# Performance work log

Measured on AMD Instinct MI355X. Metric: run time of the kernel, lower is better.

The kernel has to match this reference:

```python
import jax, jax.numpy as jnp
import numpy as np

EPS = 1e-6
K = 32
NUM_RBF = 16
NUM_PE = 16
SCALE = 30.0


def _norm(x, axis=-1):
    n = jnp.linalg.norm(x, axis=axis, keepdims=True)
    return x / jnp.maximum(n, 1e-12)


def _ln(x, g, b):
    # torch.var default is unbiased (ddof=1)
    mu = x.mean(-1, keepdims=True)
    sig = jnp.sqrt(x.var(-1, keepdims=True, ddof=1) + EPS)
    return g * (x - mu) / (sig + EPS) + b


def _gather_nodes(nodes, idx):
    # nodes [B,N,C], idx [B,N,K] -> [B,N,K,C]
    return jax.vmap(lambda nd, ei: nd[ei])(nodes, idx)


def _quat(R):
    # R [B,N,K,3,3] -> unit quaternion [B,N,K,4]
    diag = jnp.diagonal(R, axis1=-2, axis2=-1)
    Rxx, Ryy, Rzz = diag[..., 0], diag[..., 1], diag[..., 2]
    mag = 0.5 * jnp.sqrt(jnp.abs(1.0 + jnp.stack(
        [Rxx - Ryy - Rzz, -Rxx + Ryy - Rzz, -Rxx - Ryy + Rzz], -1)))
    sgn = jnp.sign(jnp.stack(
        [R[..., 2, 1] - R[..., 1, 2], R[..., 0, 2] - R[..., 2, 0], R[..., 1, 0] - R[..., 0, 1]], -1))
    w = jnp.sqrt(jax.nn.relu(1.0 + diag.sum(-1, keepdims=True))) / 2.0
    return _norm(jnp.concatenate([sgn * mag, w], -1))


def _orient(X, E_idx):
    # backbone frames + relative orientation features ('coarse')
    B = X.shape[0]
    dX = X[:, 1:] - X[:, :-1]
    U = _norm(dX)
    u2, u1, u0 = U[:, :-2], U[:, 1:-1], U[:, 2:]
    n2 = _norm(jnp.cross(u2, u1))
    n1 = _norm(jnp.cross(u1, u0))
    cosA = jnp.clip(-(u1 * u0).sum(-1), -1 + EPS, 1 - EPS)
    A = jnp.arccos(cosA)
    cosD = jnp.clip((n2 * n1).sum(-1), -1 + EPS, 1 - EPS)
    Dih = jnp.sign((u2 * n1).sum(-1)) * jnp.arccos(cosD)
    AD = jnp.stack([jnp.cos(A), jnp.sin(A) * jnp.cos(Dih), jnp.sin(A) * jnp.sin(Dih)], -1)
    AD = jnp.pad(AD, ((0, 0), (1, 2), (0, 0)))  # [B,N,3]
    o1 = _norm(u2 - u1)
    Of = jnp.stack([o1, n2, jnp.cross(o1, n2)], 2).reshape(B, -1, 9)
    Of = jnp.pad(Of, ((0, 0), (1, 2), (0, 0)))  # [B,N,9]
    O_nb = _gather_nodes(Of, E_idx).reshape(*E_idx.shape, 3, 3)
    X_nb = _gather_nodes(X, E_idx)
    Om = Of.reshape(B, -1, 3, 3)
    dU = _norm(jnp.einsum('bnij,bnkj->bnki', Om, X_nb - X[:, :, None, :]))
    R = jnp.einsum('bnji,bnkjl->bnkil', Om, O_nb)  # O^T @ O_neighbors
    return AD, jnp.concatenate([dU, _quat(R)], -1)  # [B,N,3], [B,N,K,7]


def _forward(X, mask, Wn, bn, gn, hn, We, be, ge, he, Wv, bv, Wq, bq,
             lW1, lb1, lW2, lb2, lW3, lb3, lWi, lbi, lWo, lbo, lg0, lh0, lg1, lh1):
    B, N, _ = X.shape
    # ---- kNN graph: pairwise dist + topk (smallest) ----
    mask2 = mask[:, None, :] * mask[:, :, None]
    dX = X[:, None, :, :] - X[:, :, None, :]
    D = mask2 * jnp.sqrt((dX * dX).sum(-1) + EPS)
    D_adj = D + (1.0 - mask2) * D.max(-1, keepdims=True)
    negD, E_idx = jax.lax.top_k(-D_adj, K)
    D_nb = -negD  # [B,N,K]
    # ---- edge features: positional encodings + RBF + orientations ----
    ii = jnp.arange(N, dtype=jnp.float32)[None, :, None]
    d = (E_idx.astype(jnp.float32) - ii)[..., None]
    freq = jnp.exp(jnp.arange(0, NUM_PE, 2, dtype=jnp.float32) * (-np.log(10000.0) / NUM_PE))
    ang = d * freq
    E_pos = jnp.concatenate([jnp.cos(ang), jnp.sin(ang)], -1)  # [B,N,K,16]
    mu = jnp.linspace(0.0, 20.0, NUM_RBF)
    RBF = jnp.exp(-(((D_nb[..., None] - mu) * (NUM_RBF / 20.0)) ** 2))  # [B,N,K,16]
    AD, O_feat = _orient(X, E_idx)
    # ---- embed + normalize ----
    V = _ln(AD @ Wn + bn, gn, hn)
    E = jnp.concatenate([E_pos, RBF, O_feat], -1)  # [B,N,K,39]
    E = _ln(E @ We + be, ge, he)
    h_V = V @ Wv + bv
    h_E = E @ Wq + bq
    m_att = mask[:, :, None] * _gather_nodes(mask[..., None], E_idx)[..., 0]
    # ---- MPNN layers: gather -> concat -> 3-layer MLP -> mask -> sum ----
    for l in range(lW1.shape[0]):
        h_EV = jnp.concatenate([
            jnp.broadcast_to(h_V[:, :, None, :], h_E.shape),
            h_E,
            _gather_nodes(h_V, E_idx)], -1)  # [B,N,K,3H]
        msg = jax.nn.relu(h_EV @ lW1[l] + lb1[l])
        msg = jax.nn.relu(msg @ lW2[l] + lb2[l])
        msg = (msg @ lW3[l] + lb3[l]) * m_att[..., None]
        h_V = _ln(h_V + msg.sum(-2) / SCALE, lg0[l], lh0[l])
        dh = jax.nn.relu(h_V @ lWi[l] + lbi[l]) @ lWo[l] + lbo[l]
        h_V = _ln(h_V + dh, lg1[l], lh1[l])
        h_V = mask[..., None] * h_V
    return h_V


def setup_inputs() -> dict:
    key = jax.random.key(0)
    ks = iter(jax.random.split(key, 32))
    def rn(shape, fan_in):
        return jax.random.normal(next(ks), shape, dtype=jnp.float32) / np.float32(np.sqrt(fan_in))
    H, Dff, L = 128, 512, 3
    inp = {}
    inp['X'] = jax.random.normal(next(ks), (2, 2048, 3), dtype=jnp.float32)
    inp['mask'] = jnp.ones((2, 2048), jnp.float32)
    inp['Wn'] = rn((3, H), 3);   inp['bn'] = jnp.zeros(H)
    inp['gn'] = jnp.ones(H);     inp['hn'] = jnp.zeros(H)
    inp['We'] = rn((39, H), 39); inp['be'] = jnp.zeros(H)
    inp['ge'] = jnp.ones(H);     inp['he'] = jnp.zeros(H)
    inp['Wv'] = rn((H, H), H);   inp['bv'] = jnp.zeros(H)
    inp['Wq'] = rn((H, H), H);   inp['bq'] = jnp.zeros(H)
    inp['lW1'] = rn((L, 3 * H, H), 3 * H); inp['lb1'] = jnp.zeros((L, H))
    inp['lW2'] = rn((L, H, H), H);         inp['lb2'] = jnp.zeros((L, H))
    inp['lW3'] = rn((L, H, H), H);         inp['lb3'] = jnp.zeros((L, H))
    inp['lWi'] = rn((L, H, Dff), H);       inp['lbi'] = jnp.zeros((L, Dff))
    inp['lWo'] = rn((L, Dff, H), Dff);     inp['lbo'] = jnp.zeros((L, H))
    inp['lg0'] = jnp.ones((L, H));         inp['lh0'] = jnp.zeros((L, H))
    inp['lg1'] = jnp.ones((L, H));         inp['lh1'] = jnp.zeros((L, H))
    return inp


def reference(X, mask, Wn, bn, gn, hn, We, be, ge, he, Wv, bv, Wq, bq,
              lW1, lb1, lW2, lb2, lW3, lb3, lWi, lbi, lWo, lbo, lg0, lh0, lg1, lh1):
    return _forward(X, mask, Wn, bn, gn, hn, We, be, ge, he, Wv, bv, Wq, bq,
                    lW1, lb1, lW2, lb2, lW3, lb3, lWi, lbi, lWo, lbo, lg0, lh0, lg1, lh1)
```

## Files before the change

### kernel.cpp

```cpp
#include <hip/hip_runtime.h>
#include <math.h>

typedef __attribute__((ext_vector_type(8))) short short8;
typedef __attribute__((ext_vector_type(4))) float f32x4;

#define BB 2
#define NN 2048
#define KK 32
#define HH 128
#define DFF 512
#define EPSF 1e-6f
#define INFV 1e30f

#define KNN_BLK 1024
#define PACK_BLK 2656
#define ORIENT_BLK 16

#define MFMA16(a, b, c) __builtin_amdgcn_mfma_f32_16x16x32_bf16((a), (b), (c), 0, 0, 0)


__device__ __forceinline__ unsigned short f2bf(float f) {
    unsigned u = __float_as_uint(f);
    u += 0x7fffu + ((u >> 16) & 1u);
    return (unsigned short)(u >> 16);
}

__device__ __forceinline__ float bf2f(unsigned short h) {
    return __uint_as_float(((unsigned)h) << 16);
}

__device__ __forceinline__ void f2bf2(float x, short& hi, short& lo) {
    unsigned short h = f2bf(x);
    hi = (short)h;
    lo = (short)f2bf(x - bf2f(h));
}

__device__ __forceinline__ short8 cvt8h(f32x4 a, f32x4 b) {
    short8 h8;
    #pragma unroll
    for (int i = 0; i < 4; i++) h8[i] = (short)f2bf(a[i]);
    #pragma unroll
    for (int i = 0; i < 4; i++) h8[4 + i] = (short)f2bf(b[i]);
    return h8;
}

__device__ __forceinline__ float sgnf(float x) {
    return (x > 0.f) ? 1.f : ((x < 0.f) ? -1.f : 0.f);
}

__device__ __forceinline__ void norm3(float& x, float& y, float& z) {
    float n = sqrtf(x * x + y * y + z * z);
    n = fmaxf(n, 1e-12f);
    x /= n; y /= n; z /= n;
}


__device__ void knn_body(int bid4, const float* __restrict__ X,
                         const float* __restrict__ mask,
                         int* __restrict__ E_idx,
                         float* __restrict__ D_nb) {
    int w = threadIdx.x >> 6, lane = threadIdx.x & 63;
    int g = bid4 * 4 + w;
    int b = g >> 11, n = g & 2047;
    const float* Xb = X + (size_t)b * NN * 3;
    const float* mb = mask + (size_t)b * NN;

    float xn0 = Xb[n * 3], xn1 = Xb[n * 3 + 1], xn2 = Xb[n * 3 + 2];
    float mn = mb[n];

    float Dv[32], m2a[32];
    float lmax = -1e30f;
    #pragma unroll
    for (int s = 0; s < 32; s++) {
        int j = s * 64 + lane;
        float dx = Xb[j * 3] - xn0, dy = Xb[j * 3 + 1] - xn1, dz = Xb[j * 3 + 2] - xn2;
        float d = sqrtf(dx * dx + dy * dy + dz * dz + EPSF);
        float m2 = mn * mb[j];
        float v = m2 * d;
        Dv[s] = v; m2a[s] = m2;
        lmax = fmaxf(lmax, v);
    }
    #pragma unroll
    for (int off = 1; off <= 32; off <<= 1) lmax = fmaxf(lmax, __shfl_xor(lmax, off));
    float Dmax = lmax;
    #pragma unroll
    for (int s = 0; s < 32; s++) Dv[s] += (1.f - m2a[s]) * Dmax;

    float l1 = INFV, l2 = INFV; int s1 = 0, s2 = 0;
    #pragma unroll
    for (int s = 0; s < 32; s++) {
        float v = Dv[s];
        bool lt1 = v < l1;
        bool lt2 = v < l2;
        float o1 = l1; int os1 = s1;
        l1 = lt1 ? v : l1;  s1 = lt1 ? s : s1;
        l2 = lt1 ? o1 : (lt2 ? v : l2);
        s2 = lt1 ? os1 : (lt2 ? s : s2);
    }

    unsigned used = 0u;
    float keepd = 0.f; int keepj = 0;

    for (int s = 0; s < KK; s++) {
        float m = l1;
        #pragma unroll
        for (int off = 1; off <= 32; off <<= 1) m = fminf(m, __shfl_xor(m, off));
        unsigned long long ball = __ballot(l1 == m);
        int jwin;
        if (__popcll(ball) == 1) {
            int src = (int)(__ffsll((long long)ball) - 1);
            jwin = __shfl(s1 * 64 + lane, src);
        } else {
            int jme = (l1 == m) ? (s1 * 64 + lane) : 0x7FFFFFFF;
            jwin = jme;
            #pragma unroll
            for (int off = 1; off <= 32; off <<= 1) jwin = min(jwin, __shfl_xor(jwin, off));
        }
        if (lane == s) { keepd = m; keepj = jwin; }
        if (lane == (jwin & 63)) {
            used |= 1u << s1;
            l1 = l2; s1 = s2;
            l2 = INFV;
            if (l1 >= INFV) {
                l1 = INFV; l2 = INFV;
                #pragma unroll
                for (int i = 0; i < 32; i++) {
                    float v = ((used >> i) & 1u) ? INFV : Dv[i];
                    bool lt1 = v < l1;
                    bool lt2 = v < l2;
                    float o1 = l1; int os1 = s1;
                    l1 = lt1 ? v : l1;  s1 = lt1 ? i : s1;
                    l2 = lt1 ? o1 : (lt2 ? v : l2);
                    s2 = lt1 ? os1 : (lt2 ? i : s2);
                }
            }
        }
    }
    if (lane < KK) {
        E_idx[(size_t)g * KK + lane] = keepj;
        D_nb[(size_t)g * KK + lane] = keepd;
    }
}

__device__ __forceinline__ void packB(const float* __restrict__ src, short* __restrict__ dH,
                                      short* __restrict__ dL, int e, int KC, int N, int Kreal) {
    int j = e & 7, ln = (e >> 3) & 63, t = e >> 9;
    int kc = t % KC, nt = t / KC;
    int k = kc * 32 + (ln >> 4) * 8 + j;
    int n = nt * 16 + (ln & 15);
    float v = (k < Kreal) ? src[(size_t)k * N + n] : 0.f;
    short hi, lo; f2bf2(v, hi, lo);
    dH[e] = hi; dL[e] = lo;
}

__device__ void pack_body(int e,
                          const float* __restrict__ We, const float* __restrict__ Wq,
                          const float* __restrict__ lW1, const float* __restrict__ lW2,
                          const float* __restrict__ lW3, const float* __restrict__ lWi,
                          const float* __restrict__ lWo, const float* __restrict__ Wv,
                          short* __restrict__ WeP, short* __restrict__ WqP,
                          short* __restrict__ W1bP, short* __restrict__ W2P,
                          short* __restrict__ W3P, short* __restrict__ WiP,
                          short* __restrict__ WoP, short* __restrict__ W1acP,
                          short* __restrict__ WvP) {
    if (e < 8192) { packB(We, WeP, WeP + 8192, e, 2, 128, 39); return; }
    e -= 8192;
    if (e < 16384) { packB(Wq, WqP, WqP + 16384, e, 4, 128, 128); return; }
    e -= 16384;
    if (e < 49152) {
        int l = e >> 14, r = e & 16383;
        packB(lW1 + (size_t)l * 49152 + 16384, W1bP + l * 32768, W1bP + l * 32768 + 16384, r, 4, 128, 128);
        return;
    }
    e -= 49152;
    if (e < 49152) {
        int l = e >> 14, r = e & 16383;
        packB(lW2 + (size_t)l * 16384, W2P + l * 32768, W2P + l * 32768 + 16384, r, 4, 128, 128);
        return;
    }
    e -= 49152;
    if (e < 49152) {
        int l = e >> 14, r = e & 16383;
        packB(lW3 + (size_t)l * 16384, W3P + l * 32768, W3P + l * 32768 + 16384, r, 4, 128, 128);
        return;
    }
    e -= 49152;
    if (e < 196608) {
        int l = e / 65536, r = e % 65536;
        packB(lWi + (size_t)l * 65536, WiP + l * 131072, WiP + l * 131072 + 65536, r, 4, 512, 128);
        return;
    }
    e -= 196608;
    if (e < 196608) {
        int l = e / 65536, r = e % 65536;
        packB(lWo + (size_t)l * 65536, WoP + l * 131072, WoP + l * 131072 + 65536, r, 16, 128, 512);
        return;
    }
    e -= 196608;
    if (e < 98304) {
        int l = e / 32768, r = e % 32768;
        int j = r & 7, ln = (r >> 3) & 63, t = r >> 9;
        int kc = t & 3, nt = t >> 2;
        int k = kc * 32 + (ln >> 4) * 8 + j;
        int n = nt * 16 + (ln & 15);
        const float* base = lW1 + (size_t)l * 49152;
        float v = (n < 128) ? base[(size_t)k * 128 + n] : base[(size_t)(256 + k) * 128 + (n - 128)];
        short hi, lo; f2bf2(v, hi, lo);
        short* dH = W1acP + l * 65536;
        dH[r] = hi; dH[32768 + r] = lo;
        return;
    }
    e -= 98304;
    packB(Wv, WvP, WvP + 16384, e, 4, 128, 128);
}

__device__ void orient_body(int t, const float* __restrict__ X,
                            float* __restrict__ AD, float* __restrict__ Of) {
    if (t >= BB * NN) return;
    int b = t / NN, n = t % NN;
    float* ad = AD + (size_t)t * 3;
    float* of = Of + (size_t)t * 9;
    if (n < 1 || n > NN - 3) {
        ad[0] = ad[1] = ad[2] = 0.f;
        #pragma unroll
        for (int i = 0; i < 9; i++) of[i] = 0.f;
        return;
    }
    const float* Xb = X + (size_t)b * NN * 3;
    float p0x = Xb[(n - 1) * 3], p0y = Xb[(n - 1) * 3 + 1], p0z = Xb[(n - 1) * 3 + 2];
    float p1x = Xb[n * 3],       p1y = Xb[n * 3 + 1],       p1z = Xb[n * 3 + 2];
    float p2x = Xb[(n + 1) * 3], p2y = Xb[(n + 1) * 3 + 1], p2z = Xb[(n + 1) * 3 + 2];
    float p3x = Xb[(n + 2) * 3], p3y = Xb[(n + 2) * 3 + 1], p3z = Xb[(n + 2) * 3 + 2];

    float u2x = p1x - p0x, u2y = p1y - p0y, u2z = p1z - p0z; norm3(u2x, u2y, u2z);
    float u1x = p2x - p1x, u1y = p2y - p1y, u1z = p2z - p1z; norm3(u1x, u1y, u1z);
    float u0x = p3x - p2x, u0y = p3y - p2y, u0z = p3z - p2z; norm3(u0x, u0y, u0z);

    float n2x = u2y * u1z - u2z * u1y, n2y = u2z * u1x - u2x * u1z, n2z = u2x * u1y - u2y * u1x;
    norm3(n2x, n2y, n2z);
    float n1x = u1y * u0z - u1z * u0y, n1y = u1z * u0x - u1x * u0z, n1z = u1x * u0y - u1y * u0x;
    norm3(n1x, n1y, n1z);

    float cosA = -(u1x * u0x + u1y * u0y + u1z * u0z);
    cosA = fminf(fmaxf(cosA, -1.f + EPSF), 1.f - EPSF);
    float A = acosf(cosA);
    float cosD = n2x * n1x + n2y * n1y + n2z * n1z;
    cosD = fminf(fmaxf(cosD, -1.f + EPSF), 1.f - EPSF);
    float sg = sgnf(u2x * n1x + u2y * n1y + u2z * n1z);
    float Dih = sg * acosf(cosD);

    ad[0] = cosf(A);
    ad[1] = sinf(A) * cosf(Dih);
    ad[2] = sinf(A) * sinf(Dih);

    float o1x = u2x - u1x, o1y = u2y - u1y, o1z = u2z - u1z; norm3(o1x, o1y, o1z);
    float cx = o1y * n2z - o1z * n2y, cy = o1z * n2x - o1x * n2z, cz = o1x * n2y - o1y * n2x;
    of[0] = o1x; of[1] = o1y; of[2] = o1z;
    of[3] = n2x; of[4] = n2y; of[5] = n2z;
    of[6] = cx;  of[7] = cy;  of[8] = cz;
}


__global__ __launch_bounds__(256) void front_kernel(const float* __restrict__ X,
                                                    const float* __restrict__ mask,
                                                    int* __restrict__ E_idx,
                                                    float* __restrict__ D_nb,
                                                    const float* __restrict__ We,
                                                    const float* __restrict__ Wq,
                                                    const float* __restrict__ lW1,
                                                    const float* __restrict__ lW2,
                                                    const float* __restrict__ lW3,
                                                    const float* __restrict__ lWi,
                                                    const float* __restrict__ lWo,
                                                    const float* __restrict__ Wv,
                                                    short* __restrict__ WeP,
                                                    short* __restrict__ WqP,
                                                    short* __restrict__ W1bP,
                                                    short* __restrict__ W2P,
                                                    short* __restrict__ W3P,
                                                    short* __restrict__ WiP,
                                                    short* __restrict__ WoP,
                                                    short* __restrict__ W1acP,
                                                    short* __restrict__ WvP,
                                                    float* __restrict__ ADb,
                                                    float* __restrict__ Ofb) {
    int blk = blockIdx.x;
    if (blk < KNN_BLK) {
        knn_body(blk, X, mask, E_idx, D_nb);
    } else if (blk < KNN_BLK + PACK_BLK) {
        pack_body((blk - KNN_BLK) * 256 + threadIdx.x,
                  We, Wq, lW1, lW2, lW3, lWi, lWo, Wv,
                  WeP, WqP, W1bP, W2P, W3P, WiP, WoP, W1acP, WvP);
    } else {
        orient_body((blk - KNN_BLK - PACK_BLK) * 256 + threadIdx.x, X, ADb, Ofb);
    }
}


__global__ __launch_bounds__(128) void mid_kernel(const float* __restrict__ X,
                                                  const int* __restrict__ E_idx,
                                                  const float* __restrict__ D_nb,
                                                  const float* __restrict__ Of,
                                                  const float* __restrict__ be,
                                                  const float* __restrict__ ge,
                                                  const float* __restrict__ he,
                                                  const float* __restrict__ bq,
                                                  const short* __restrict__ WeP,
                                                  const short* __restrict__ WqP,
                                                  unsigned short* __restrict__ hEbH,
                                                  const float* __restrict__ AD,
                                                  const float* __restrict__ Wn,
                                                  const float* __restrict__ bn,
                                                  const float* __restrict__ gn,
                                                  const float* __restrict__ hn,
                                                  const short* __restrict__ WvP,
                                                  const float* __restrict__ bv,
                                                  const short* __restrict__ W1acP0,
                                                  const float* __restrict__ b1_0,
                                                  float* __restrict__ hV,
                                                  float* __restrict__ P,
                                                  float* __restrict__ Q) {
    __shared__ __align__(16) char smemRaw[15872];

    if (blockIdx.x < (unsigned)(BB * NN)) {
        short* AefH = (short*)smemRaw;
        short* AeH  = (short*)(smemRaw + 4608);
        float* beS  = (float*)(smemRaw + 13312);
        float* geS  = beS + HH;
        float* heS  = geS + HH;
        float* bqS  = heS + HH;
        float* redSe = (float*)(smemRaw + 15360);

        int bid = blockIdx.x; int b = bid >> 11, n = bid & 2047; int tid = threadIdx.x;
        int lane = tid & 63, w = tid >> 6;
        beS[tid] = be[tid]; geS[tid] = ge[tid]; heS[tid] = he[tid]; bqS[tid] = bq[tid];
        {
            unsigned* Az = (unsigned*)AefH;
            for (int i = tid; i < 32 * 72 / 2; i += 128) Az[i] = 0u;
        }
        __syncthreads();

        int part = tid >> 5, k = tid & 31;
        int e = E_idx[(size_t)bid * KK + k];
        float dpos = (float)e - (float)n;
        if (part == 1 || part == 2) {
            int p0 = (part - 1) * 4;
            #pragma unroll
            for (int p = 0; p < 4; p++) {
                float fr = (part == 1)
                    ? ((p == 0) ? 1.f : (p == 1) ? 0.31622776601683794f
                       : (p == 2) ? 0.1f : 0.031622776601683791f)
                    : ((p == 0) ? 0.01f : (p == 1) ? 0.0031622776601683794f
                       : (p == 2) ? 0.001f : 0.00031622776601683794f);
                float ang = dpos * fr;
                AefH[k * 72 + p0 + p]     = (short)f2bf(__cosf(ang));
                AefH[k * 72 + 8 + p0 + p] = (short)f2bf(__sinf(ang));
            }
        } else if (part == 3) {
            float Dv = D_nb[(size_t)bid * KK + k];
            #pragma unroll
            for (int i = 0; i < 16; i++) {
                float m = (20.f / 15.f) * (float)i;
                float z = (Dv - m) * 0.8f;
                AefH[k * 72 + 16 + i] = (short)f2bf(__expf(-z * z));
            }
        } else {
            const float* Omp = Of + (size_t)(b * NN + n) * 9;
            const float* Onp = Of + (size_t)(b * NN + e) * 9;
            float Om[9], On[9];
            #pragma unroll
            for (int i = 0; i < 9; i++) { Om[i] = Omp[i]; On[i] = Onp[i]; }
            float vx = X[(size_t)(b * NN + e) * 3 + 0] - X[(size_t)(b * NN + n) * 3 + 0];
            float vy = X[(size_t)(b * NN + e) * 3 + 1] - X[(size_t)(b * NN + n) * 3 + 1];
            float vz = X[(size_t)(b * NN + e) * 3 + 2] - X[(size_t)(b * NN + n) * 3 + 2];
            float t0 = Om[0] * vx + Om[1] * vy + Om[2] * vz;
            float t1 = Om[3] * vx + Om[4] * vy + Om[5] * vz;
            float t2 = Om[6] * vx + Om[7] * vy + Om[8] * vz;
            float nr = fmaxf(sqrtf(t0 * t0 + t1 * t1 + t2 * t2), 1e-12f);
            AefH[k * 72 + 32] = (short)f2bf(t0 / nr);
            AefH[k * 72 + 33] = (short)f2bf(t1 / nr);
            AefH[k * 72 + 34] = (short)f2bf(t2 / nr);
            float R[9];
            #pragma unroll
            for (int i = 0; i < 3; i++)
                #pragma unroll
                for (int l = 0; l < 3; l++)
                    R[i * 3 + l] = Om[0 + i] * On[0 + l] + Om[3 + i] * On[3 + l] + Om[6 + i] * On[6 + l];
            float Rxx = R[0], Ryy = R[4], Rzz = R[8];
            float mx = 0.5f * sqrtf(fabsf(1.f + Rxx - Ryy - Rzz));
            float my = 0.5f * sqrtf(fabsf(1.f - Rxx + Ryy - Rzz));
            float mz = 0.5f * sqrtf(fabsf(1.f - Rxx - Ryy + Rzz));
            float qx = sgnf(R[7] - R[5]) * mx;
            float qy = sgnf(R[2] - R[6]) * my;
            float qz = sgnf(R[3] - R[1]) * mz;
            float qw = 0.5f * sqrtf(fmaxf(1.f + Rxx + Ryy + Rzz, 0.f));
            float qn = fmaxf(sqrtf(qx * qx + qy * qy + qz * qz + qw * qw), 1e-12f);
            AefH[k * 72 + 35] = (short)f2bf(qx / qn);
            AefH[k * 72 + 36] = (short)f2bf(qy / qn);
            AefH[k * 72 + 37] = (short)f2bf(qz / qn);
            AefH[k * 72 + 38] = (short)f2bf(qw / qn);
        }
        __syncthreads();

        int m = lane & 15, q = lane >> 4;
        short8 aW[2][2];
        #pragma unroll
        for (int t = 0; t < 2; t++) {
            int row = (t * 16 + m) * 72;
            aW[t][0] = *(const short8*)&AefH[row + q * 8];
            aW[t][1] = *(const short8*)&AefH[row + 32 + q * 8];
        }
        f32x4 accA[4][2];
        #pragma unroll
        for (int nt4 = 0; nt4 < 4; nt4++) {
            int ntg = w * 4 + nt4;
            const short* B0 = &WeP[((ntg * 2 + 0) * 64 + lane) * 8];
            const short* B1 = &WeP[((ntg * 2 + 1) * 64 + lane) * 8];
            short8 b0h = *(const short8*)B0, b0l = *(const short8*)(B0 + 8192);
            short8 b1h = *(const short8*)B1, b1l = *(const short8*)(B1 + 8192);
            float bc = beS[ntg * 16 + m];
            #pragma unroll
            for (int t = 0; t < 2; t++) {
                f32x4 acc = {bc, bc, bc, bc};
                acc = MFMA16(aW[t][0], b0h, acc);
                acc = MFMA16(aW[t][0], b0l, acc);
                acc = MFMA16(aW[t][1], b1h, acc);
                acc = MFMA16(aW[t][1], b1l, acc);
                accA[nt4][t] = acc;
            }
        }
        #pragma unroll
        for (int t = 0; t < 2; t++)
            #pragma unroll
            for (int r = 0; r < 4; r++) {
                float su = accA[0][t][r] + accA[1][t][r] + accA[2][t][r] + accA[3][t][r];
                float sq2 = accA[0][t][r] * accA[0][t][r] + accA[1][t][r] * accA[1][t][r]
                          + accA[2][t][r] * accA[2][t][r] + accA[3][t][r] * accA[3][t][r];
                #pragma unroll
                for (int off = 1; off <= 8; off <<= 1) {
                    su += __shfl_xor(su, off); sq2 += __shfl_xor(sq2, off);
                }
                if (m == 0) {
                    int row = t * 16 + q * 4 + r;
                    redSe[(w * 2 + 0) * 32 + row] = su;
                    redSe[(w * 2 + 1) * 32 + row] = sq2;
                }
            }
        __syncthreads();
        float muA[2][4], invA[2][4];
        #pragma unroll
        for (int t = 0; t < 2; t++)
            #pragma unroll
            for (int r = 0; r < 4; r++) {
                int row = t * 16 + q * 4 + r;
                float S  = redSe[0 * 32 + row] + redSe[2 * 32 + row];
                float Q2 = redSe[1 * 32 + row] + redSe[3 * 32 + row];
                float mu = S * (1.f / HH);
                float var = (Q2 - (float)HH * mu * mu) * (1.f / (HH - 1));
                muA[t][r] = mu;
                invA[t][r] = 1.f / (sqrtf(var + EPSF) + EPSF);
            }
        #pragma unroll
        for (int nt4 = 0; nt4 < 4; nt4++) {
            int col = (w * 4 + nt4) * 16 + m;
            float g = geS[col], hh = heS[col];
            #pragma unroll
            for (int t = 0; t < 2; t++)
                #pragma unroll
                for (int r = 0; r < 4; r++) {
                    int edge = t * 16 + q * 4 + r;
                    float y = g * (accA[nt4][t][r] - muA[t][r]) * invA[t][r] + hh;
                    AeH[edge * 136 + col] = (short)f2bf(y);
                }
        }
        __syncthreads();

        short8 ah[2][4];
        #pragma unroll
        for (int t = 0; t < 2; t++)
            #pragma unroll
            for (int kc = 0; kc < 4; kc++)
                ah[t][kc] = *(const short8*)&AeH[(t * 16 + m) * 136 + kc * 32 + q * 8];
        #pragma unroll
        for (int nt4 = 0; nt4 < 4; nt4++) {
            int ntg = w * 4 + nt4;
            int col = ntg * 16 + m;
            short8 qh[4], ql[4];
            #pragma unroll
            for (int kc = 0; kc < 4; kc++) {
                const short* Bp = &WqP[((ntg * 4 + kc) * 64 + lane) * 8];
                qh[kc] = *(const short8*)Bp;
                ql[kc] = *(const short8*)(Bp + 16384);
            }
            float bc = bqS[col];
            #pragma unroll
            for (int t = 0; t < 2; t++) {
                f32x4 acc = {bc, bc, bc, bc};
                #pragma unroll
                for (int kc = 0; kc < 4; kc++) {
                    acc = MFMA16(ah[t][kc], qh[kc], acc);
                    acc = MFMA16(ah[t][kc], ql[kc], acc);
                }
                #pragma unroll
                for (int r = 0; r < 4; r++) {
                    int edge = t * 16 + q * 4 + r;
                    hEbH[(size_t)bid * (KK * HH) + edge * HH + col] = f2bf(acc[r]);
                }
            }
        }
    } else {
        short* yH  = (short*)smemRaw;
        short* hvH = (short*)(smemRaw + 4352);

        int nb = blockIdx.x - BB * NN;
        int g0 = nb * 16;
        int tid = threadIdx.x;
        int lane = tid & 63, w = tid >> 6;
        int m = lane & 15, q = lane >> 4;

        {
            int i = tid >> 3;
            int j = tid & 7;
            int h0 = j * 16;
            const float* ad = AD + (size_t)(g0 + i) * 3;
            float a0 = ad[0], a1 = ad[1], a2 = ad[2];
            float v[16];
            float su = 0.f, sq = 0.f;
            #pragma unroll
            for (int c = 0; c < 16; c++) {
                int h = h0 + c;
                float t = bn[h] + a0 * Wn[h] + a1 * Wn[HH + h] + a2 * Wn[2 * HH + h];
                v[c] = t; su += t; sq += t * t;
            }
            #pragma unroll
            for (int off = 1; off <= 4; off <<= 1) {
                su += __shfl_xor(su, off); sq += __shfl_xor(sq, off);
            }
            float mu = su * (1.f / HH);
            float var = (sq - (float)HH * mu * mu) * (1.f / (HH - 1));
            float inv = 1.f / (sqrtf(var + EPSF) + EPSF);
            #pragma unroll
            for (int c = 0; c < 16; c++) {
                int h = h0 + c;
                yH[i * 136 + h] = (short)f2bf(gn[h] * (v[c] - mu) * inv + hn[h]);
            }
        }
        __syncthreads();

        short8 ayh[4];
        #pragma unroll
        for (int kc = 0; kc < 4; kc++)
            ayh[kc] = *(const short8*)&yH[m * 136 + kc * 32 + q * 8];
        #pragma unroll
        for (int u = 0; u < 4; u++) {
            int nt = w * 4 + u;
            int col = nt * 16 + m;
            float bc = bv[col];
            f32x4 a = {bc, bc, bc, bc};
            #pragma unroll
            for (int kc = 0; kc < 4; kc++) {
                const short* Bp = &WvP[((nt * 4 + kc) * 64 + lane) * 8];
                short8 bh = *(const short8*)Bp, bl = *(const short8*)(Bp + 16384);
                a = MFMA16(ayh[kc], bh, a);
                a = MFMA16(ayh[kc], bl, a);
            }
            #pragma unroll
            for (int r = 0; r < 4; r++) {
                int rw = q * 4 + r;
                hV[(size_t)(g0 + rw) * HH + col] = a[r];
                hvH[rw * 136 + col] = (short)f2bf(a[r]);
            }
        }
        __syncthreads();

        short8 avh[4];
        #pragma unroll
        for (int kc = 0; kc < 4; kc++)
            avh[kc] = *(const short8*)&hvH[m * 136 + kc * 32 + q * 8];
        #pragma unroll
        for (int u = 0; u < 8; u++) {
            int nt = w * 8 + u;
            int col = nt * 16 + m;
            float b0 = (nt < 8) ? b1_0[col] : 0.f;
            f32x4 a = {b0, b0, b0, b0};
            #pragma unroll
            for (int kc = 0; kc < 4; kc++) {
                const short* Bp = &W1acP0[((nt * 4 + kc) * 64 + lane) * 8];
                short8 bh = *(const short8*)Bp, bl = *(const short8*)(Bp + 32768);
                a = MFMA16(avh[kc], bh, a);
                a = MFMA16(avh[kc], bl, a);
            }
            #pragma unroll
            for (int r = 0; r < 4; r++) {
                size_t rw = g0 + q * 4 + r;
                if (nt < 8) P[rw * HH + col] = a[r];
                else        Q[rw * HH + (col - 128)] = a[r];
            }
        }
    }
}


__global__ __launch_bounds__(128) void msg_kernel(const float* __restrict__ mask,
                                                  const int* __restrict__ E_idx,
                                                  const unsigned short* __restrict__ hEbH,
                                                  const float* __restrict__ P,
                                                  const float* __restrict__ Q,
                                                  const short* __restrict__ W1bP,
                                                  const short* __restrict__ W2P,
                                                  const float* __restrict__ b2,
                                                  float* __restrict__ sOut,
                                                  float* __restrict__ cntOut) {
    __shared__ short stg[2][32 * 136];
    __shared__ short AmH[2][32 * 136];

    int tid = threadIdx.x;
    int w = tid >> 6, lane = tid & 63;
    int gA = blockIdx.x * 2;
    int b = gA >> 11;
    int m = lane & 15, q = lane >> 4;

    {
        const short8* src = (const short8*)(hEbH + (size_t)gA * (KK * HH));
        #pragma unroll
        for (int it = 0; it < 8; it++) {
            int idx = it * 128 + tid;
            int nd = idx >> 9;
            int rem = idx & 511;
            int e = rem >> 4;
            int c8 = rem & 15;
            short8 v = src[idx];
            *(short8*)&stg[nd][e * 136 + c8 * 8] = v;
        }
    }

    int qbase[2][2][4]; float mt[2][2][4];
    #pragma unroll
    for (int nd = 0; nd < 2; nd++) {
        float maskv = mask[gA + nd];
        #pragma unroll
        for (int t = 0; t < 2; t++)
            #pragma unroll
            for (int r = 0; r < 4; r++) {
                int row = t * 16 + q * 4 + r;
                int e = E_idx[(size_t)(gA + nd) * KK + row];
                qbase[nd][t][r] = (b * NN + e) * HH;
                mt[nd][t][r] = maskv * mask[b * NN + e];
            }
    }
    {
        float c8 = mt[w][0][0] + mt[w][0][1] + mt[w][0][2] + mt[w][0][3]
                 + mt[w][1][0] + mt[w][1][1] + mt[w][1][2] + mt[w][1][3];
        c8 += __shfl_xor(c8, 16);
        c8 += __shfl_xor(c8, 32);
        if (lane == 0) cntOut[gA + w] = c8;
    }

    float preg[2][4], b2reg[4];
    #pragma unroll
    for (int nt4 = 0; nt4 < 4; nt4++) {
        int colg = (w * 4 + nt4) * 16 + m;
        b2reg[nt4] = b2[colg];
        preg[0][nt4] = P[(size_t)gA * HH + colg];
        preg[1][nt4] = P[(size_t)(gA + 1) * HH + colg];
    }
    __syncthreads();

    #pragma unroll
    for (int nt4 = 0; nt4 < 4; nt4++) {
        int ntg = w * 4 + nt4;
        int colg = ntg * 16 + m;
        short8 bh[4], bl[4];
        #pragma unroll
        for (int kc = 0; kc < 4; kc++) {
            const short* Bp = &W1bP[((ntg * 4 + kc) * 64 + lane) * 8];
            bh[kc] = *(const short8*)Bp;
            bl[kc] = *(const short8*)(Bp + 16384);
        }
        #pragma unroll
        for (int nd = 0; nd < 2; nd++) {
            f32x4 t0 = {0.f, 0.f, 0.f, 0.f}, t1 = {0.f, 0.f, 0.f, 0.f};
            #pragma unroll
            for (int kc = 0; kc < 4; kc++) {
                short8 a0 = *(const short8*)&stg[nd][(0 * 16 + m) * 136 + kc * 32 + q * 8];
                short8 a1 = *(const short8*)&stg[nd][(1 * 16 + m) * 136 + kc * 32 + q * 8];
                t0 = MFMA16(a0, bh[kc], t0);
                t0 = MFMA16(a0, bl[kc], t0);
                t1 = MFMA16(a1, bh[kc], t1);
                t1 = MFMA16(a1, bl[kc], t1);
            }
            float pp = preg[nd][nt4];
            #pragma unroll
            for (int r = 0; r < 4; r++) {
                float v0 = fmaxf(t0[r] + pp + Q[(size_t)qbase[nd][0][r] + colg], 0.f);
                AmH[nd][(q * 4 + r) * 136 + colg] = (short)f2bf(v0);
                float v1 = fmaxf(t1[r] + pp + Q[(size_t)qbase[nd][1][r] + colg], 0.f);
                AmH[nd][(16 + q * 4 + r) * 136 + colg] = (short)f2bf(v1);
            }
        }
    }
    __syncthreads();

    #pragma unroll
    for (int nt4 = 0; nt4 < 4; nt4++) {
        int ntg = w * 4 + nt4;
        short8 bh[4], bl[4];
        #pragma unroll
        for (int kc = 0; kc < 4; kc++) {
            const short* Bp = &W2P[((ntg * 4 + kc) * 64 + lane) * 8];
            bh[kc] = *(const short8*)Bp;
            bl[kc] = *(const short8*)(Bp + 16384);
        }
        float bc = b2reg[nt4];
        #pragma unroll
        for (int nd = 0; nd < 2; nd++) {
            f32x4 a0 = {bc, bc, bc, bc}, a1 = {bc, bc, bc, bc};
            #pragma unroll
            for (int kc = 0; kc < 4; kc++) {
                short8 m0 = *(const short8*)&AmH[nd][(0 * 16 + m) * 136 + kc * 32 + q * 8];
                short8 m1 = *(const short8*)&AmH[nd][(1 * 16 + m) * 136 + kc * 32 + q * 8];
                a0 = MFMA16(m0, bh[kc], a0);
                a0 = MFMA16(m0, bl[kc], a0);
                a1 = MFMA16(m1, bh[kc], a1);
                a1 = MFMA16(m1, bl[kc], a1);
            }
            float part = 0.f;
            #pragma unroll
            for (int r = 0; r < 4; r++)
                part += fmaxf(a0[r], 0.f) * mt[nd][0][r] + fmaxf(a1[r], 0.f) * mt[nd][1][r];
            part += __shfl_xor(part, 16);
            part += __shfl_xor(part, 32);
            if (q == 0) sOut[(size_t)(gA + nd) * HH + ntg * 16 + m] = part;
        }
    }
}


#define HSTR 520

__global__ __launch_bounds__(256, 3) void node_kernel(const float* __restrict__ mask,
                                                      const float* __restrict__ sbuf,
                                                      const float* __restrict__ cntb,
                                                      const float* __restrict__ hVin,
                                                      const short* __restrict__ W3P,
                                                      const float* __restrict__ b3,
                                                      const short* __restrict__ WiP,
                                                      const float* __restrict__ biN,
                                                      const short* __restrict__ WoP,
                                                      const float* __restrict__ boN,
                                                      const float* __restrict__ g0,
                                                      const float* __restrict__ h0,
                                                      const float* __restrict__ g1,
                                                      const float* __restrict__ h1,
                                                      const short* __restrict__ W1P,
                                                      const float* __restrict__ b1n,
                                                      float* __restrict__ hVout,
                                                      float* __restrict__ Pn,
                                                      float* __restrict__ Qn) {
    __shared__ short rbH[16 * 136];
    __shared__ short hbH[16 * HSTR];
    __shared__ float redS[4][2][16];
    __shared__ float g0S[128], h0S[128], g1S[128], h1S[128], b3S[128], boS[128], b1S[128];
    __shared__ float biS[512];

    int tid = threadIdx.x;
    int w = tid >> 6, lane = tid & 63;
    int m = lane & 15, q = lane >> 4;
    int rowT = blockIdx.x * 16;

    for (int i = tid; i < 128; i += 256) {
        g0S[i] = g0[i]; h0S[i] = h0[i]; g1S[i] = g1[i]; h1S[i] = h1[i];
        b3S[i] = b3[i]; boS[i] = boN[i]; b1S[i] = W1P ? b1n[i] : 0.f;
    }
    for (int i = tid; i < 512; i += 256) biS[i] = biN[i];
    __syncthreads();

    short8 ash[4];
    #pragma unroll
    for (int kc = 0; kc < 4; kc++) {
        const float* sp = &sbuf[(size_t)(rowT + m) * HH + kc * 32 + q * 8];
        f32x4 x0 = *(const f32x4*)sp;
        f32x4 x1 = *(const f32x4*)(sp + 4);
        ash[kc] = cvt8h(x0, x1);
    }
    float cntr[4];
    #pragma unroll
    for (int r = 0; r < 4; r++) cntr[r] = cntb[rowT + q * 4 + r];

    f32x4 vC2[2];
    #pragma unroll
    for (int t = 0; t < 2; t++) {
        int nt = 2 * w + t;
        f32x4 a = {0.f, 0.f, 0.f, 0.f};
        #pragma unroll
        for (int kc = 0; kc < 4; kc++) {
            const short* Bp = &W3P[((nt * 4 + kc) * 64 + lane) * 8];
            short8 bh = *(const short8*)Bp, bl = *(const short8*)(Bp + 16384);
            a = MFMA16(ash[kc], bh, a);
            a = MFMA16(ash[kc], bl, a);
        }
        int col = nt * 16 + m;
        #pragma unroll
        for (int r = 0; r < 4; r++) {
            float tv = (a[r] + cntr[r] * b3S[col]) * (1.f / 30.f);
            a[r] = hVin[(size_t)(rowT + q * 4 + r) * HH + col] + tv;
        }
        vC2[t] = a;
    }

    {
        float su[4] = {0, 0, 0, 0}, sq[4] = {0, 0, 0, 0};
        #pragma unroll
        for (int t = 0; t < 2; t++)
            #pragma unroll
            for (int r = 0; r < 4; r++) { float v = vC2[t][r]; su[r] += v; sq[r] += v * v; }
        #pragma unroll
        for (int off = 1; off <= 8; off <<= 1)
            #pragma unroll
            for (int r = 0; r < 4; r++) { su[r] += __shfl_xor(su[r], off); sq[r] += __shfl_xor(sq[r], off); }
        if (m == 0) {
            #pragma unroll
            for (int r = 0; r < 4; r++) { redS[w][0][q * 4 + r] = su[r]; redS[w][1][q * 4 + r] = sq[r]; }
        }
    }
    __syncthreads();
    float mu[4], inv[4];
    #pragma unroll
    for (int r = 0; r < 4; r++) {
        int row = q * 4 + r;
        float S  = redS[0][0][row] + redS[1][0][row] + redS[2][0][row] + redS[3][0][row];
        float Q2 = redS[0][1][row] + redS[1][1][row] + redS[2][1][row] + redS[3][1][row];
        mu[r] = S * (1.f / HH);
        float var = (Q2 - (float)HH * mu[r] * mu[r]) * (1.f / (HH - 1));
        inv[r] = 1.f / (sqrtf(var + EPSF) + EPSF);
    }
    #pragma unroll
    for (int t = 0; t < 2; t++) {
        int col = (2 * w + t) * 16 + m;
        #pragma unroll
        for (int r = 0; r < 4; r++)
            vC2[t][r] = g0S[col] * (vC2[t][r] - mu[r]) * inv[r] + h0S[col];
    }
    #pragma unroll
    for (int t = 0; t < 2; t++) {
        int col = (2 * w + t) * 16 + m;
        #pragma unroll
        for (int r = 0; r < 4; r++)
            rbH[(q * 4 + r) * 136 + col] = (short)f2bf(vC2[t][r]);
    }
    __syncthreads();

    short8 avh[4];
    #pragma unroll
    for (int kc = 0; kc < 4; kc++)
        avh[kc] = *(const short8*)&rbH[m * 136 + kc * 32 + q * 8];

    #pragma unroll
    for (int nt2 = 0; nt2 < 8; nt2++) {
        int jcol = w * 128 + nt2 * 16 + m;
        float bb = biS[jcol];
        f32x4 a = {bb, bb, bb, bb};
        #pragma unroll
        for (int kc = 0; kc < 4; kc++) {
            const short* Bp = &WiP[(((w * 8 + nt2) * 4 + kc) * 64 + lane) * 8];
            short8 bh = *(const short8*)Bp, bl = *(const short8*)(Bp + 65536);
            a = MFMA16(avh[kc], bh, a);
            a = MFMA16(avh[kc], bl, a);
        }
        #pragma unroll
        for (int r = 0; r < 4; r++)
            hbH[(q * 4 + r) * HSTR + jcol] = (short)f2bf(fmaxf(a[r], 0.f));
    }
    __syncthreads();

    f32x4 oC2[2] = {{0.f, 0.f, 0.f, 0.f}, {0.f, 0.f, 0.f, 0.f}};
    for (int kc2 = 0; kc2 < 16; kc2++) {
        short8 ahh = *(const short8*)&hbH[m * HSTR + kc2 * 32 + q * 8];
        #pragma unroll
        for (int t = 0; t < 2; t++) {
            int nt = 2 * w + t;
            const short* Bp = &WoP[((nt * 16 + kc2) * 64 + lane) * 8];
            short8 bh = *(const short8*)Bp, bl = *(const short8*)(Bp + 65536);
            oC2[t] = MFMA16(ahh, bh, oC2[t]);
            oC2[t] = MFMA16(ahh, bl, oC2[t]);
        }
    }
    #pragma unroll
    for (int t = 0; t < 2; t++) {
        int col = (2 * w + t) * 16 + m;
        #pragma unroll
        for (int r = 0; r < 4; r++)
            oC2[t][r] += boS[col] + vC2[t][r];
    }

    {
        float su[4] = {0, 0, 0, 0}, sq[4] = {0, 0, 0, 0};
        #pragma unroll
        for (int t = 0; t < 2; t++)
            #pragma unroll
            for (int r = 0; r < 4; r++) { float v = oC2[t][r]; su[r] += v; sq[r] += v * v; }
        #pragma unroll
        for (int off = 1; off <= 8; off <<= 1)
            #pragma unroll
            for (int r = 0; r < 4; r++) { su[r] += __shfl_xor(su[r], off); sq[r] += __shfl_xor(sq[r], off); }
        __syncthreads();
        if (m == 0) {
            #pragma unroll
            for (int r = 0; r < 4; r++) { redS[w][0][q * 4 + r] = su[r]; redS[w][1][q * 4 + r] = sq[r]; }
        }
    }
    __syncthreads();
    #pragma unroll
    for (int r = 0; r < 4; r++) {
        int row = q * 4 + r;
        float S  = redS[0][0][row] + redS[1][0][row] + redS[2][0][row] + redS[3][0][row];
        float Q2 = redS[0][1][row] + redS[1][1][row] + redS[2][1][row] + redS[3][1][row];
        mu[r] = S * (1.f / HH);
        float var = (Q2 - (float)HH * mu[r] * mu[r]) * (1.f / (HH - 1));
        inv[r] = 1.f / (sqrtf(var + EPSF) + EPSF);
    }
    float mk[4];
    #pragma unroll
    for (int r = 0; r < 4; r++) mk[r] = mask[rowT + q * 4 + r];
    #pragma unroll
    for (int t = 0; t < 2; t++) {
        int col = (2 * w + t) * 16 + m;
        #pragma unroll
        for (int r = 0; r < 4; r++) {
            float y = g1S[col] * (oC2[t][r] - mu[r]) * inv[r] + h1S[col];
            y *= mk[r];
            oC2[t][r] = y;
            hVout[(size_t)(rowT + q * 4 + r) * HH + col] = y;
        }
    }

    if (W1P) {
        __syncthreads();
        #pragma unroll
        for (int t = 0; t < 2; t++) {
            int col = (2 * w + t) * 16 + m;
            #pragma unroll
            for (int r = 0; r < 4; r++)
                rbH[(q * 4 + r) * 136 + col] = (short)f2bf(oC2[t][r]);
        }
        __syncthreads();
        short8 ayh[4];
        #pragma unroll
        for (int kc = 0; kc < 4; kc++)
            ayh[kc] = *(const short8*)&rbH[m * 136 + kc * 32 + q * 8];
        #pragma unroll
        for (int u = 0; u < 4; u++) {
            int nt = w * 4 + u;
            int col = nt * 16 + m;
            float b0 = (nt < 8) ? b1S[col] : 0.f;
            f32x4 a = {b0, b0, b0, b0};
            #pragma unroll
            for (int kc = 0; kc < 4; kc++) {
                const short* Bp = &W1P[((nt * 4 + kc) * 64 + lane) * 8];
                short8 bh = *(const short8*)Bp, bl = *(const short8*)(Bp + 32768);
                a = MFMA16(ayh[kc], bh, a);
                a = MFMA16(ayh[kc], bl, a);
            }
            #pragma unroll
            for (int r = 0; r < 4; r++) {
                size_t row = rowT + q * 4 + r;
                if (nt < 8) Pn[row * HH + col] = a[r];
                else        Qn[row * HH + (col - 128)] = a[r];
            }
        }
    }
}


extern "C" void kernel_launch(void* const* d_in, const int* in_sizes, int n_in,
                              void* d_out, int out_size, void* d_ws, size_t ws_size,
                              hipStream_t stream) {
    const float* X    = (const float*)d_in[0];
    const float* mask = (const float*)d_in[1];
    const float* Wn   = (const float*)d_in[2];
    const float* bn   = (const float*)d_in[3];
    const float* gn   = (const float*)d_in[4];
    const float* hn   = (const float*)d_in[5];
    const float* We   = (const float*)d_in[6];
    const float* be   = (const float*)d_in[7];
    const float* ge   = (const float*)d_in[8];
    const float* he   = (const float*)d_in[9];
    const float* Wv   = (const float*)d_in[10];
    const float* bv   = (const float*)d_in[11];
    const float* Wq   = (const float*)d_in[12];
    const float* bq   = (const float*)d_in[13];
    const float* lW1  = (const float*)d_in[14];
    const float* lb1  = (const float*)d_in[15];
    const float* lW2  = (const float*)d_in[16];
    const float* lb2  = (const float*)d_in[17];
    const float* lW3  = (const float*)d_in[18];
    const float* lb3  = (const float*)d_in[19];
    const float* lWi  = (const float*)d_in[20];
    const float* lbi  = (const float*)d_in[21];
    const float* lWo  = (const float*)d_in[22];
    const float* lbo  = (const float*)d_in[23];
    const float* lg0  = (const float*)d_in[24];
    const float* lh0  = (const float*)d_in[25];
    const float* lg1  = (const float*)d_in[26];
    const float* lh1  = (const float*)d_in[27];

    char* ws = (char*)d_ws;
    size_t off = 0;
    auto alloc = [&](size_t nbytes) { void* p = ws + off; off += (nbytes + 15) & ~(size_t)15; return p; };
    int*   E_idx = (int*)  alloc((size_t)BB * NN * KK * 4);
    float* D_nb  = (float*)alloc((size_t)BB * NN * KK * 4);
    float* ADb   = (float*)alloc((size_t)BB * NN * 3 * 4);
    float* Ofb   = (float*)alloc((size_t)BB * NN * 9 * 4);
    float* hV    = (float*)alloc((size_t)BB * NN * HH * 4);
    unsigned short* hEbH = (unsigned short*)alloc((size_t)BB * NN * KK * HH * 2);
    float* Pb    = (float*)alloc((size_t)BB * NN * HH * 4);
    float* Qb    = (float*)alloc((size_t)BB * NN * HH * 4);
    float* sBuf  = (float*)alloc((size_t)BB * NN * HH * 4);
    float* cntB  = (float*)alloc((size_t)BB * NN * 4);
    short* WeP   = (short*)alloc(2 * 8192 * 2);
    short* WqP   = (short*)alloc(2 * 16384 * 2);
    short* W1bP  = (short*)alloc(3 * 2 * 16384 * 2);
    short* W2P   = (short*)alloc(3 * 2 * 16384 * 2);
    short* W3P   = (short*)alloc(3 * 2 * 16384 * 2);
    short* WiP   = (short*)alloc(3 * 2 * 65536 * 2);
    short* WoP   = (short*)alloc(3 * 2 * 65536 * 2);
    short* W1acP = (short*)alloc(3 * 2 * 32768 * 2);
    short* WvP   = (short*)alloc(2 * 16384 * 2);
    if (off > ws_size) return;

    front_kernel<<<KNN_BLK + PACK_BLK + ORIENT_BLK, 256, 0, stream>>>(
        X, mask, E_idx, D_nb,
        We, Wq, lW1, lW2, lW3, lWi, lWo, Wv,
        WeP, WqP, W1bP, W2P, W3P, WiP, WoP, W1acP, WvP,
        ADb, Ofb);

    mid_kernel<<<BB * NN + BB * NN / 16, 128, 0, stream>>>(
        X, E_idx, D_nb, Ofb, be, ge, he, bq, WeP, WqP, hEbH,
        ADb, Wn, bn, gn, hn, WvP, bv, W1acP, lb1, hV, Pb, Qb);

    for (int l = 0; l < 3; l++) {
        int last = (l == 2);
        msg_kernel<<<BB * NN / 2, HH, 0, stream>>>(
            mask, E_idx, hEbH, Pb, Qb,
            W1bP + (size_t)l * 32768,
            W2P + (size_t)l * 32768, lb2 + (size_t)l * HH,
            sBuf, cntB);
        node_kernel<<<BB * NN / 16, 256, 0, stream>>>(
            mask, sBuf, cntB, hV,
            W3P + (size_t)l * 32768, lb3 + (size_t)l * HH,
            WiP + (size_t)l * 131072, lbi + (size_t)l * DFF,
            WoP + (size_t)l * 131072, lbo + (size_t)l * HH,
            lg0 + (size_t)l * HH, lh0 + (size_t)l * HH,
            lg1 + (size_t)l * HH, lh1 + (size_t)l * HH,
            last ? nullptr : (W1acP + (size_t)(l + 1) * 65536),
            last ? nullptr : (lb1 + (size_t)(l + 1) * HH),
            last ? (float*)d_out : hV,
            Pb, Qb);
    }
}
```

Before: 359.6 us.

## Use 8 waves per block in node kernel, one 16-column tile per wave

Doubles the node_kernel block from 256 to 512 threads, so each of 8 waves now owns a single 16-column output tile instead of two. Every GEMM stage (W3, Wi, Wo, W1) and both layer-norm reductions are repartitioned to match, with the reduction buffer widened to 8 waves. The aim is more wave-level parallelism and fewer registers per thread, giving each block more latency hiding. The cost is more waves contending at each barrier and a lower block occupancy bound (2 blocks per CU).

```diff
diff --git a/kernel.cpp b/kernel.cpp
--- a/kernel.cpp
+++ b/kernel.cpp
@@ -738,7 +738,7 @@
 
 #define HSTR 520
 
-__global__ __launch_bounds__(256, 3) void node_kernel(const float* __restrict__ mask,
+__global__ __launch_bounds__(512, 2) void node_kernel(const float* __restrict__ mask,
                                                       const float* __restrict__ sbuf,
                                                       const float* __restrict__ cntb,
                                                       const float* __restrict__ hVin,
@@ -759,7 +759,7 @@
                                                       float* __restrict__ Qn) {
     __shared__ short rbH[16 * 136];
     __shared__ short hbH[16 * HSTR];
-    __shared__ float redS[4][2][16];
+    __shared__ float redS[8][2][16];
     __shared__ float g0S[128], h0S[128], g1S[128], h1S[128], b3S[128], boS[128], b1S[128];
     __shared__ float biS[512];
 
@@ -768,11 +768,12 @@
     int m = lane & 15, q = lane >> 4;
     int rowT = blockIdx.x * 16;
 
-    for (int i = tid; i < 128; i += 256) {
+    if (tid < 128) {
+        int i = tid;
         g0S[i] = g0[i]; h0S[i] = h0[i]; g1S[i] = g1[i]; h1S[i] = h1[i];
         b3S[i] = b3[i]; boS[i] = boN[i]; b1S[i] = W1P ? b1n[i] : 0.f;
     }
-    for (int i = tid; i < 512; i += 256) biS[i] = biN[i];
+    biS[tid] = biN[tid];
     __syncthreads();
 
     short8 ash[4];
@@ -787,33 +788,29 @@
     #pragma unroll
     for (int r = 0; r < 4; r++) cntr[r] = cntb[rowT + q * 4 + r];
 
-    f32x4 vC2[2];
-    #pragma unroll
-    for (int t = 0; t < 2; t++) {
-        int nt = 2 * w + t;
+    f32x4 vC;
+    {
         f32x4 a = {0.f, 0.f, 0.f, 0.f};
         #pragma unroll
         for (int kc = 0; kc < 4; kc++) {
-            const short* Bp = &W3P[((nt * 4 + kc) * 64 + lane) * 8];
+            const short* Bp = &W3P[((w * 4 + kc) * 64 + lane) * 8];
             short8 bh = *(const short8*)Bp, bl = *(const short8*)(Bp + 16384);
             a = MFMA16(ash[kc], bh, a);
             a = MFMA16(ash[kc], bl, a);
         }
-        int col = nt * 16 + m;
+        int col = w * 16 + m;
         #pragma unroll
         for (int r = 0; r < 4; r++) {
             float tv = (a[r] + cntr[r] * b3S[col]) * (1.f / 30.f);
             a[r] = hVin[(size_t)(rowT + q * 4 + r) * HH + col] + tv;
         }
-        vC2[t] = a;
+        vC = a;
     }
 
     {
-        float su[4] = {0, 0, 0, 0}, sq[4] = {0, 0, 0, 0};
-        #pragma unroll
-        for (int t = 0; t < 2; t++)
-            #pragma unroll
-            for (int r = 0; r < 4; r++) { float v = vC2[t][r]; su[r] += v; sq[r] += v * v; }
+        float su[4], sq[4];
+        #pragma unroll
+        for (int r = 0; r < 4; r++) { float v = vC[r]; su[r] = v; sq[r] = v * v; }
         #pragma unroll
         for (int off = 1; off <= 8; off <<= 1)
             #pragma unroll
@@ -828,25 +825,20 @@
     #pragma unroll
     for (int r = 0; r < 4; r++) {
         int row = q * 4 + r;
-        float S  = redS[0][0][row] + redS[1][0][row] + redS[2][0][row] + redS[3][0][row];
-        float Q2 = redS[0][1][row] + redS[1][1][row] + redS[2][1][row] + redS[3][1][row];
+        float S = 0.f, Q2 = 0.f;
+        #pragma unroll
+        for (int ww = 0; ww < 8; ww++) { S += redS[ww][0][row]; Q2 += redS[ww][1][row]; }
         mu[r] = S * (1.f / HH);
         float var = (Q2 - (float)HH * mu[r] * mu[r]) * (1.f / (HH - 1));
         inv[r] = 1.f / (sqrtf(var + EPSF) + EPSF);
     }
-    #pragma unroll
-    for (int t = 0; t < 2; t++) {
-        int col = (2 * w + t) * 16 + m;
-        #pragma unroll
-        for (int r = 0; r < 4; r++)
-            vC2[t][r] = g0S[col] * (vC2[t][r] - mu[r]) * inv[r] + h0S[col];
-    }
-    #pragma unroll
-    for (int t = 0; t < 2; t++) {
-        int col = (2 * w + t) * 16 + m;
-        #pragma unroll
-        for (int r = 0; r < 4; r++)
-            rbH[(q * 4 + r) * 136 + col] = (short)f2bf(vC2[t][r]);
+    {
+        int col = w * 16 + m;
+        #pragma unroll
+        for (int r = 0; r < 4; r++) {
+            vC[r] = g0S[col] * (vC[r] - mu[r]) * inv[r] + h0S[col];
+            rbH[(q * 4 + r) * 136 + col] = (short)f2bf(vC[r]);
+        }
     }
     __syncthreads();
 
@@ -856,13 +848,14 @@
         avh[kc] = *(const short8*)&rbH[m * 136 + kc * 32 + q * 8];
 
     #pragma unroll
-    for (int nt2 = 0; nt2 < 8; nt2++) {
-        int jcol = w * 128 + nt2 * 16 + m;
+    for (int u = 0; u < 4; u++) {
+        int nt = w * 4 + u;
+        int jcol = nt * 16 + m;
         float bb = biS[jcol];
         f32x4 a = {bb, bb, bb, bb};
         #pragma unroll
         for (int kc = 0; kc < 4; kc++) {
-            const short* Bp = &WiP[(((w * 8 + nt2) * 4 + kc) * 64 + lane) * 8];
+            const short* Bp = &WiP[((nt * 4 + kc) * 64 + lane) * 8];
             short8 bh = *(const short8*)Bp, bl = *(const short8*)(Bp + 65536);
             a = MFMA16(avh[kc], bh, a);
             a = MFMA16(avh[kc], bl, a);
@@ -873,32 +866,25 @@
     }
     __syncthreads();
 
-    f32x4 oC2[2] = {{0.f, 0.f, 0.f, 0.f}, {0.f, 0.f, 0.f, 0.f}};
+    f32x4 oC = {0.f, 0.f, 0.f, 0.f};
     for (int kc2 = 0; kc2 < 16; kc2++) {
         short8 ahh = *(const short8*)&hbH[m * HSTR + kc2 * 32 + q * 8];
-        #pragma unroll
-        for (int t = 0; t < 2; t++) {
-            int nt = 2 * w + t;
-            const short* Bp = &WoP[((nt * 16 + kc2) * 64 + lane) * 8];
-            short8 bh = *(const short8*)Bp, bl = *(const short8*)(Bp + 65536);
-            oC2[t] = MFMA16(ahh, bh, oC2[t]);
-            oC2[t] = MFMA16(ahh, bl, oC2[t]);
-        }
-    }
-    #pragma unroll
-    for (int t = 0; t < 2; t++) {
-        int col = (2 * w + t) * 16 + m;
+        const short* Bp = &WoP[((w * 16 + kc2) * 64 + lane) * 8];
+        short8 bh = *(const short8*)Bp, bl = *(const short8*)(Bp + 65536);
+        oC = MFMA16(ahh, bh, oC);
+        oC = MFMA16(ahh, bl, oC);
+    }
+    {
+        int col = w * 16 + m;
         #pragma unroll
         for (int r = 0; r < 4; r++)
-            oC2[t][r] += boS[col] + vC2[t][r];
+            oC[r] += boS[col] + vC[r];
     }
 
     {
-        float su[4] = {0, 0, 0, 0}, sq[4] = {0, 0, 0, 0};
-        #pragma unroll
-        for (int t = 0; t < 2; t++)
-            #pragma unroll
-            for (int r = 0; r < 4; r++) { float v = oC2[t][r]; su[r] += v; sq[r] += v * v; }
+        float su[4], sq[4];
+        #pragma unroll
+        for (int r = 0; r < 4; r++) { float v = oC[r]; su[r] = v; sq[r] = v * v; }
         #pragma unroll
         for (int off = 1; off <= 8; off <<= 1)
             #pragma unroll
@@ -913,8 +899,9 @@
     #pragma unroll
     for (int r = 0; r < 4; r++) {
         int row = q * 4 + r;
-        float S  = redS[0][0][row] + redS[1][0][row] + redS[2][0][row] + redS[3][0][row];
-        float Q2 = redS[0][1][row] + redS[1][1][row] + redS[2][1][row] + redS[3][1][row];
+        float S = 0.f, Q2 = 0.f;
+        #pragma unroll
+        for (int ww = 0; ww < 8; ww++) { S += redS[ww][0][row]; Q2 += redS[ww][1][row]; }
         mu[r] = S * (1.f / HH);
         float var = (Q2 - (float)HH * mu[r] * mu[r]) * (1.f / (HH - 1));
         inv[r] = 1.f / (sqrtf(var + EPSF) + EPSF);
@@ -922,26 +909,24 @@
     float mk[4];
     #pragma unroll
     for (int r = 0; r < 4; r++) mk[r] = mask[rowT + q * 4 + r];
-    #pragma unroll
-    for (int t = 0; t < 2; t++) {
-        int col = (2 * w + t) * 16 + m;
+    {
+        int col = w * 16 + m;
         #pragma unroll
         for (int r = 0; r < 4; r++) {
-            float y = g1S[col] * (oC2[t][r] - mu[r]) * inv[r] + h1S[col];
+            float y = g1S[col] * (oC[r] - mu[r]) * inv[r] + h1S[col];
             y *= mk[r];
-            oC2[t][r] = y;
+            oC[r] = y;
             hVout[(size_t)(rowT + q * 4 + r) * HH + col] = y;
         }
     }
 
     if (W1P) {
         __syncthreads();
-        #pragma unroll
-        for (int t = 0; t < 2; t++) {
-            int col = (2 * w + t) * 16 + m;
+        {
+            int col = w * 16 + m;
             #pragma unroll
             for (int r = 0; r < 4; r++)
-                rbH[(q * 4 + r) * 136 + col] = (short)f2bf(oC2[t][r]);
+                rbH[(q * 4 + r) * 136 + col] = (short)f2bf(oC[r]);
         }
         __syncthreads();
         short8 ayh[4];
@@ -949,8 +934,8 @@
         for (int kc = 0; kc < 4; kc++)
             ayh[kc] = *(const short8*)&rbH[m * 136 + kc * 32 + q * 8];
         #pragma unroll
-        for (int u = 0; u < 4; u++) {
-            int nt = w * 4 + u;
+        for (int u = 0; u < 2; u++) {
+            int nt = w * 2 + u;
             int col = nt * 16 + m;
             float b0 = (nt < 8) ? b1S[col] : 0.f;
             f32x4 a = {b0, b0, b0, b0};
@@ -1045,7 +1030,7 @@
             W1bP + (size_t)l * 32768,
             W2P + (size_t)l * 32768, lb2 + (size_t)l * HH,
             sBuf, cntB);
-        node_kernel<<<BB * NN / 16, 256, 0, stream>>>(
+        node_kernel<<<BB * NN / 16, 512, 0, stream>>>(
             mask, sBuf, cntB, hV,
             W3P + (size_t)l * 32768, lb3 + (size_t)l * HH,
             WiP + (size_t)l * 131072, lbi + (size_t)l * DFF,
```

Result: faster. 324.7 us (-9.7%).
